# Kernel optimization log

Hardware: AMD Instinct MI355X
Metric: run time of the kernel (lower is better)

The kernel has to match this reference:

```python
import jax, jax.numpy as jnp
import numpy as np
from math import sqrt

SCALE = sqrt(512.0)  # max(key_size, attn_hidden_size, query_size) with scaled=True

def setup_inputs() -> dict:
    key = jax.random.key(0)
    k1, k2, k3, k4, k5 = jax.random.split(key, 5)
    B, T, S, M, N, H = 8, 512, 512, 512, 512, 128
    return {
        "query": jax.random.normal(k1, (B, T, M), dtype=jnp.float32),
        "keys": jax.random.normal(k2, (B, S, N), dtype=jnp.float32),
        "W1": jax.random.normal(k3, (N, H), dtype=jnp.float32),
        "W2": jax.random.normal(k4, (M, H), dtype=jnp.float32),
        "v": jax.random.normal(k5, (H,), dtype=jnp.float32),
    }

def reference(query, keys, W1, W2, v):
    # Project query and keys into attention hidden space
    x1 = jnp.einsum('btm,mh->bth', query, W2)   # (B,T,H)
    x2 = jnp.einsum('bsn,nh->bsh', keys, W1)    # (B,S,H)
    # Broadcast merge (op='add'), tanh activation, v-weighted reduction over H
    merged = jnp.tanh(x1[:, :, None, :] + x2[:, None, :, :])  # (B,T,S,H)
    score = jnp.einsum('btsh,h->bts', merged, v)
    return score / SCALE
```

## Files before the change

### kernel.cpp

```cpp
#include <hip/hip_runtime.h>
#include <hip/hip_fp16.h>


constexpr float SCALE_IN  = 2.8853900817779268f;
constexpr float INV_SCALE = 0.04419417382415922f;

__global__ __launch_bounds__(512) void proj_kernel(
    const float* __restrict__ q,  const float* __restrict__ w2,
    const float* __restrict__ ky, const float* __restrict__ w1,
    unsigned int* __restrict__ x1w, unsigned int* __restrict__ x2w) {
  __shared__ float As[32 * 64];
  __shared__ float Ws[64 * 128];

  int blk = blockIdx.x;
  const float* A; const float* W; unsigned int* O;
  if (blk < 128) { A = q;  W = w2; O = x1w; }
  else           { blk -= 128; A = ky; W = w1; O = x2w; }
  const int rbase = blk * 32;
  const int tid = threadIdx.x;

  const int rq = tid >> 5;
  const int hq = tid & 31;

  float acc[2][4];
#pragma unroll
  for (int r = 0; r < 2; ++r)
#pragma unroll
    for (int c = 0; c < 4; ++c) acc[r][c] = 0.0f;

  for (int kb = 0; kb < 512; kb += 64) {
    {
      const int arow = tid >> 4;
      const int kq4  = (tid & 15) * 4;
      *(float4*)(As + arow * 64 + kq4) =
          *(const float4*)(A + (size_t)(rbase + arow) * 512 + kb + kq4);
      const int wrow = tid >> 5;
      const int hq4  = (tid & 31) * 4;
#pragma unroll
      for (int p = 0; p < 4; ++p)
        *(float4*)(Ws + (wrow + 16 * p) * 128 + hq4) =
            *(const float4*)(W + (size_t)(kb + wrow + 16 * p) * 128 + hq4);
    }
    __syncthreads();
#pragma unroll 4
    for (int k4 = 0; k4 < 64; k4 += 4) {
      float a[2][4], w[4][4];
      *(float4*)a[0] = *(const float4*)(As + (2 * rq + 0) * 64 + k4);
      *(float4*)a[1] = *(const float4*)(As + (2 * rq + 1) * 64 + k4);
#pragma unroll
      for (int kk = 0; kk < 4; ++kk)
        *(float4*)w[kk] = *(const float4*)(Ws + (k4 + kk) * 128 + 4 * hq);
#pragma unroll
      for (int kk = 0; kk < 4; ++kk)
#pragma unroll
        for (int r = 0; r < 2; ++r)
#pragma unroll
          for (int c = 0; c < 4; ++c)
            acc[r][c] = fmaf(a[r][kk], w[kk][c], acc[r][c]);
    }
    __syncthreads();
  }

#pragma unroll
  for (int r = 0; r < 2; ++r) {
    unsigned int pk[4];
#pragma unroll
    for (int c = 0; c < 4; ++c) {
      const float z  = acc[r][c] * SCALE_IN;
      const float kf = rintf(z);
      const int   ki = (int)kf;
      const float em = __builtin_amdgcn_exp2f(z - kf);
      const __half hh = __float2half_rn(em);
      pk[c] = ((unsigned int)ki << 16) | (unsigned int)__half_as_ushort(hh);
    }
    *(uint4*)(O + (size_t)(rbase + 2 * rq + r) * 128 + 4 * hq) = *(uint4*)pk;
  }
}

__global__ __launch_bounds__(512) void score_kernel(
    const unsigned int* __restrict__ x1w, const unsigned int* __restrict__ x2w,
    const float* __restrict__ v, float* __restrict__ out) {
  __shared__ unsigned int x1l[128 * 64];
  __shared__ unsigned int x2l[128 * 64];

  const int tid   = threadIdx.x;
  const int b     = blockIdx.x >> 6;
  const int tile  = blockIdx.x & 63;
  const int tbase = (tile >> 3) * 64;
  const int sbase = (tile & 7) * 64;

  const uint4* x1g = (const uint4*)(x1w + (b * 512 + tbase) * 128);
  const uint4* x2g = (const uint4*)(x2w + (b * 512 + sbase) * 128);

  const int l  = tid & 63;
  const int wq = tid >> 6;
#pragma unroll
  for (int p = 0; p < 4; ++p) {
    const int row = (l & 31) + 32 * (p & 1);
    const int c4  = (l >> 5) + 2 * wq + 16 * (p >> 1);
    const uint4 a = x1g[row * 32 + c4];
    x1l[(4 * c4 + 0) * 64 + row] = a.x;
    x1l[(4 * c4 + 1) * 64 + row] = a.y;
    x1l[(4 * c4 + 2) * 64 + row] = a.z;
    x1l[(4 * c4 + 3) * 64 + row] = a.w;
    const uint4 c = x2g[row * 32 + c4];
    x2l[(4 * c4 + 0) * 64 + row] = c.x;
    x2l[(4 * c4 + 1) * 64 + row] = c.y;
    x2l[(4 * c4 + 2) * 64 + row] = c.z;
    x2l[(4 * c4 + 3) * 64 + row] = c.w;
  }
  __syncthreads();

  const int sg = tid & 15;
  const int tg = tid >> 4;

  float racc[2][4];
#pragma unroll
  for (int i = 0; i < 2; ++i)
#pragma unroll
    for (int j = 0; j < 4; ++j) racc[i][j] = 0.0f;
  float sv = 0.0f;

  for (int hg = 0; hg < 32; ++hg) {
    const int h0 = hg * 4;
    const float4 vq = *(const float4*)(v + h0);
    sv += (vq.x + vq.y) + (vq.z + vq.w);

    float emt[2][4]; int kt[2][4];
    float ems[4][4]; int ks[4][4];
#pragma unroll
    for (int qq = 0; qq < 4; ++qq) {
      const uint2 tp = *(const uint2*)(x1l + (h0 + qq) * 64 + 2 * tg);
      emt[0][qq] = __half2float(__ushort_as_half((unsigned short)tp.x));
      kt [0][qq] = ((int)tp.x) >> 16;
      emt[1][qq] = __half2float(__ushort_as_half((unsigned short)tp.y));
      kt [1][qq] = ((int)tp.y) >> 16;
      const uint4 sp = *(const uint4*)(x2l + (h0 + qq) * 64 + 4 * sg);
      ems[0][qq] = __half2float(__ushort_as_half((unsigned short)sp.x));
      ks [0][qq] = ((int)sp.x) >> 16;
      ems[1][qq] = __half2float(__ushort_as_half((unsigned short)sp.y));
      ks [1][qq] = ((int)sp.y) >> 16;
      ems[2][qq] = __half2float(__ushort_as_half((unsigned short)sp.z));
      ks [2][qq] = ((int)sp.z) >> 16;
      ems[3][qq] = __half2float(__ushort_as_half((unsigned short)sp.w));
      ks [3][qq] = ((int)sp.w) >> 16;
    }

#pragma unroll
    for (int i = 0; i < 2; ++i) {
#pragma unroll
      for (int j = 0; j < 4; ++j) {
        float e[4];
#pragma unroll
        for (int qq = 0; qq < 4; ++qq) {
          int kk = kt[i][qq] + ks[j][qq];
          kk = min(kk, 30);
          e[qq] = ldexpf(emt[i][qq] * ems[j][qq], kk);
        }
        const float a0 = e[0] + 1.0f, a1 = e[1] + 1.0f;
        const float a2 = e[2] + 1.0f, a3 = e[3] + 1.0f;
        const float p12 = a0 * a1, p34 = a2 * a3;
        float u1 = vq.x * a1; u1 = fmaf(vq.y, a0, u1);
        float u2 = vq.z * a3; u2 = fmaf(vq.w, a2, u2);
        float num = u1 * p34; num = fmaf(u2, p12, num);
        const float den = p12 * p34;
        racc[i][j] = fmaf(num, __builtin_amdgcn_rcpf(den), racc[i][j]);
      }
    }
  }

  const float c1 = sv * INV_SCALE;
  const float c2 = -2.0f * INV_SCALE;
#pragma unroll
  for (int i = 0; i < 2; ++i) {
    const int t = tbase + 2 * tg + i;
    float4 o;
    o.x = fmaf(racc[i][0], c2, c1);
    o.y = fmaf(racc[i][1], c2, c1);
    o.z = fmaf(racc[i][2], c2, c1);
    o.w = fmaf(racc[i][3], c2, c1);
    *(float4*)(out + (size_t)(b * 512 + t) * 512 + sbase + 4 * sg) = o;
  }
}

extern "C" void kernel_launch(void* const* d_in, const int* in_sizes, int n_in,
                              void* d_out, int out_size, void* d_ws, size_t ws_size,
                              hipStream_t stream) {
  const float* query = (const float*)d_in[0];
  const float* keys  = (const float*)d_in[1];
  const float* W1    = (const float*)d_in[2];
  const float* W2    = (const float*)d_in[3];
  const float* v     = (const float*)d_in[4];
  float* out = (float*)d_out;

  unsigned int* x1w = (unsigned int*)d_ws;
  unsigned int* x2w = x1w + 8 * 512 * 128;

  hipLaunchKernelGGL(proj_kernel, dim3(256), dim3(512), 0, stream,
                     query, W2, keys, W1, x1w, x2w);
  hipLaunchKernelGGL(score_kernel, dim3(512), dim3(512), 0, stream,
                     x1w, x2w, v, out);
}
```

Measured before the change: 145.7 us.

## Pack score math into float2 vectors and retile kernels to smaller blocks

```diff
diff --git a/kernel.cpp b/kernel.cpp
--- a/kernel.cpp
+++ b/kernel.cpp
@@ -2,25 +2,26 @@
 #include <hip/hip_fp16.h>
 
 
+typedef float vf2 __attribute__((ext_vector_type(2)));
+
 constexpr float SCALE_IN  = 2.8853900817779268f;
 constexpr float INV_SCALE = 0.04419417382415922f;
 
-__global__ __launch_bounds__(512) void proj_kernel(
+__global__ __launch_bounds__(256) void proj_kernel(
     const float* __restrict__ q,  const float* __restrict__ w2,
     const float* __restrict__ ky, const float* __restrict__ w1,
     unsigned int* __restrict__ x1w, unsigned int* __restrict__ x2w) {
-  __shared__ float As[32 * 64];
+  __shared__ float As[16 * 64];
   __shared__ float Ws[64 * 128];
 
   int blk = blockIdx.x;
   const float* A; const float* W; unsigned int* O;
-  if (blk < 128) { A = q;  W = w2; O = x1w; }
-  else           { blk -= 128; A = ky; W = w1; O = x2w; }
-  const int rbase = blk * 32;
+  if (blk < 256) { A = q;  W = w2; O = x1w; }
+  else           { blk -= 256; A = ky; W = w1; O = x2w; }
+  const int rbase = blk * 16;
   const int tid = threadIdx.x;
-
-  const int rq = tid >> 5;
-  const int hq = tid & 31;
+  const int hq  = tid & 31;
+  const int rg  = tid >> 5;
 
   float acc[2][4];
 #pragma unroll
@@ -31,22 +32,22 @@
   for (int kb = 0; kb < 512; kb += 64) {
     {
       const int arow = tid >> 4;
-      const int kq4  = (tid & 15) * 4;
-      *(float4*)(As + arow * 64 + kq4) =
-          *(const float4*)(A + (size_t)(rbase + arow) * 512 + kb + kq4);
-      const int wrow = tid >> 5;
-      const int hq4  = (tid & 31) * 4;
-#pragma unroll
-      for (int p = 0; p < 4; ++p)
-        *(float4*)(Ws + (wrow + 16 * p) * 128 + hq4) =
-            *(const float4*)(W + (size_t)(kb + wrow + 16 * p) * 128 + hq4);
+      const int k4   = (tid & 15) * 4;
+      *(float4*)(As + arow * 64 + k4) =
+          *(const float4*)(A + (size_t)(rbase + arow) * 512 + kb + k4);
+      const int hq4 = (tid & 31) * 4;
+      const int w0  = tid >> 5;
+#pragma unroll
+      for (int p = 0; p < 8; ++p)
+        *(float4*)(Ws + (w0 + 8 * p) * 128 + hq4) =
+            *(const float4*)(W + (size_t)(kb + w0 + 8 * p) * 128 + hq4);
     }
     __syncthreads();
 #pragma unroll 4
     for (int k4 = 0; k4 < 64; k4 += 4) {
       float a[2][4], w[4][4];
-      *(float4*)a[0] = *(const float4*)(As + (2 * rq + 0) * 64 + k4);
-      *(float4*)a[1] = *(const float4*)(As + (2 * rq + 1) * 64 + k4);
+      *(float4*)a[0] = *(const float4*)(As + (2 * rg + 0) * 64 + k4);
+      *(float4*)a[1] = *(const float4*)(As + (2 * rg + 1) * 64 + k4);
 #pragma unroll
       for (int kk = 0; kk < 4; ++kk)
         *(float4*)w[kk] = *(const float4*)(Ws + (k4 + kk) * 128 + 4 * hq);
@@ -70,101 +71,107 @@
       const float kf = rintf(z);
       const int   ki = (int)kf;
       const float em = __builtin_amdgcn_exp2f(z - kf);
-      const __half hh = __float2half_rn(em);
-      pk[c] = ((unsigned int)ki << 16) | (unsigned int)__half_as_ushort(hh);
-    }
-    *(uint4*)(O + (size_t)(rbase + 2 * rq + r) * 128 + 4 * hq) = *(uint4*)pk;
+      pk[c] = ((unsigned int)ki << 16) |
+              (unsigned int)__half_as_ushort(__float2half_rn(em));
+    }
+    *(uint4*)(O + (size_t)(rbase + 2 * rg + r) * 128 + 4 * hq) = *(uint4*)pk;
   }
 }
 
-__global__ __launch_bounds__(512) void score_kernel(
+__global__ __launch_bounds__(256) void score_kernel(
     const unsigned int* __restrict__ x1w, const unsigned int* __restrict__ x2w,
     const float* __restrict__ v, float* __restrict__ out) {
-  __shared__ unsigned int x1l[128 * 64];
-  __shared__ unsigned int x2l[128 * 64];
+  __shared__ unsigned int x1l[64 * 64];
+  __shared__ unsigned int x2l[64 * 32];
 
   const int tid   = threadIdx.x;
-  const int b     = blockIdx.x >> 6;
-  const int tile  = blockIdx.x & 63;
-  const int tbase = (tile >> 3) * 64;
-  const int sbase = (tile & 7) * 64;
-
-  const uint4* x1g = (const uint4*)(x1w + (b * 512 + tbase) * 128);
-  const uint4* x2g = (const uint4*)(x2w + (b * 512 + sbase) * 128);
-
-  const int l  = tid & 63;
-  const int wq = tid >> 6;
-#pragma unroll
-  for (int p = 0; p < 4; ++p) {
-    const int row = (l & 31) + 32 * (p & 1);
-    const int c4  = (l >> 5) + 2 * wq + 16 * (p >> 1);
-    const uint4 a = x1g[row * 32 + c4];
-    x1l[(4 * c4 + 0) * 64 + row] = a.x;
-    x1l[(4 * c4 + 1) * 64 + row] = a.y;
-    x1l[(4 * c4 + 2) * 64 + row] = a.z;
-    x1l[(4 * c4 + 3) * 64 + row] = a.w;
-    const uint4 c = x2g[row * 32 + c4];
-    x2l[(4 * c4 + 0) * 64 + row] = c.x;
-    x2l[(4 * c4 + 1) * 64 + row] = c.y;
-    x2l[(4 * c4 + 2) * 64 + row] = c.z;
-    x2l[(4 * c4 + 3) * 64 + row] = c.w;
-  }
-  __syncthreads();
+  const int b     = blockIdx.x >> 7;
+  const int tile  = blockIdx.x & 127;
+  const int tbase = (tile >> 4) * 64;
+  const int sbase = (tile & 15) * 32;
 
   const int sg = tid & 15;
   const int tg = tid >> 4;
 
-  float racc[2][4];
-#pragma unroll
-  for (int i = 0; i < 2; ++i)
-#pragma unroll
-    for (int j = 0; j < 4; ++j) racc[i][j] = 0.0f;
+  const int st_t = tid >> 2, st_q = tid & 3;
+  const int s2_t = tid >> 3, s2_q = tid & 7;
+
+  const uint4* x1g = (const uint4*)x1w + (size_t)(b * 512 + tbase) * 32;
+  const uint4* x2g = (const uint4*)x2w + (size_t)(b * 512 + sbase) * 32;
+
+  vf2 racc[4];
+#pragma unroll
+  for (int i = 0; i < 4; ++i) racc[i] = (vf2){0.0f, 0.0f};
   float sv = 0.0f;
 
-  for (int hg = 0; hg < 32; ++hg) {
-    const int h0 = hg * 4;
-    const float4 vq = *(const float4*)(v + h0);
-    sv += (vq.x + vq.y) + (vq.z + vq.w);
-
-    float emt[2][4]; int kt[2][4];
-    float ems[4][4]; int ks[4][4];
-#pragma unroll
-    for (int qq = 0; qq < 4; ++qq) {
-      const uint2 tp = *(const uint2*)(x1l + (h0 + qq) * 64 + 2 * tg);
-      emt[0][qq] = __half2float(__ushort_as_half((unsigned short)tp.x));
-      kt [0][qq] = ((int)tp.x) >> 16;
-      emt[1][qq] = __half2float(__ushort_as_half((unsigned short)tp.y));
-      kt [1][qq] = ((int)tp.y) >> 16;
-      const uint4 sp = *(const uint4*)(x2l + (h0 + qq) * 64 + 4 * sg);
-      ems[0][qq] = __half2float(__ushort_as_half((unsigned short)sp.x));
-      ks [0][qq] = ((int)sp.x) >> 16;
-      ems[1][qq] = __half2float(__ushort_as_half((unsigned short)sp.y));
-      ks [1][qq] = ((int)sp.y) >> 16;
-      ems[2][qq] = __half2float(__ushort_as_half((unsigned short)sp.z));
-      ks [2][qq] = ((int)sp.z) >> 16;
-      ems[3][qq] = __half2float(__ushort_as_half((unsigned short)sp.w));
-      ks [3][qq] = ((int)sp.w) >> 16;
-    }
-
-#pragma unroll
-    for (int i = 0; i < 2; ++i) {
-#pragma unroll
-      for (int j = 0; j < 4; ++j) {
-        float e[4];
+  for (int c = 0; c < 2; ++c) {
+    if (c) __syncthreads();
+#pragma unroll
+    for (int p = 0; p < 4; ++p) {
+      const int hq = st_q + 4 * p;
+      const uint4 a = x1g[(size_t)st_t * 32 + 16 * c + hq];
+      x1l[(4 * hq + 0) * 64 + st_t] = a.x;
+      x1l[(4 * hq + 1) * 64 + st_t] = a.y;
+      x1l[(4 * hq + 2) * 64 + st_t] = a.z;
+      x1l[(4 * hq + 3) * 64 + st_t] = a.w;
+    }
+#pragma unroll
+    for (int p = 0; p < 2; ++p) {
+      const int hq = s2_q + 8 * p;
+      const uint4 a = x2g[(size_t)s2_t * 32 + 16 * c + hq];
+      x2l[(4 * hq + 0) * 32 + s2_t] = a.x;
+      x2l[(4 * hq + 1) * 32 + s2_t] = a.y;
+      x2l[(4 * hq + 2) * 32 + s2_t] = a.z;
+      x2l[(4 * hq + 3) * 32 + s2_t] = a.w;
+    }
+    __syncthreads();
+
+    for (int hg = 0; hg < 16; ++hg) {
+      const int h0 = 4 * hg;
+      const float4 vq = *(const float4*)(v + 64 * c + h0);
+      sv += (vq.x + vq.y) + (vq.z + vq.w);
+
+      float emt[4][4]; int kt[4][4];
+      vf2 ems[4]; int ks[4][2];
+#pragma unroll
+      for (int qq = 0; qq < 4; ++qq) {
+        const uint4 tp = *(const uint4*)(x1l + (h0 + qq) * 64 + 4 * tg);
+        emt[qq][0] = __half2float(__ushort_as_half((unsigned short)tp.x));
+        kt [qq][0] = ((int)tp.x) >> 16;
+        emt[qq][1] = __half2float(__ushort_as_half((unsigned short)tp.y));
+        kt [qq][1] = ((int)tp.y) >> 16;
+        emt[qq][2] = __half2float(__ushort_as_half((unsigned short)tp.z));
+        kt [qq][2] = ((int)tp.z) >> 16;
+        emt[qq][3] = __half2float(__ushort_as_half((unsigned short)tp.w));
+        kt [qq][3] = ((int)tp.w) >> 16;
+        const uint2 sp = *(const uint2*)(x2l + (h0 + qq) * 32 + 2 * sg);
+        ems[qq].x = __half2float(__ushort_as_half((unsigned short)sp.x));
+        ems[qq].y = __half2float(__ushort_as_half((unsigned short)sp.y));
+        ks [qq][0] = ((int)sp.x) >> 16;
+        ks [qq][1] = ((int)sp.y) >> 16;
+      }
+
+#pragma unroll
+      for (int i = 0; i < 4; ++i) {
+        vf2 Aq[4];
 #pragma unroll
         for (int qq = 0; qq < 4; ++qq) {
-          int kk = kt[i][qq] + ks[j][qq];
-          kk = min(kk, 30);
-          e[qq] = ldexpf(emt[i][qq] * ems[j][qq], kk);
+          const int k0 = min(kt[qq][i] + ks[qq][0], 30);
+          const int k1 = min(kt[qq][i] + ks[qq][1], 30);
+          const vf2 m = emt[qq][i] * ems[qq];
+          vf2 e; e.x = ldexpf(m.x, k0); e.y = ldexpf(m.y, k1);
+          Aq[qq] = e + 1.0f;
         }
-        const float a0 = e[0] + 1.0f, a1 = e[1] + 1.0f;
-        const float a2 = e[2] + 1.0f, a3 = e[3] + 1.0f;
-        const float p12 = a0 * a1, p34 = a2 * a3;
-        float u1 = vq.x * a1; u1 = fmaf(vq.y, a0, u1);
-        float u2 = vq.z * a3; u2 = fmaf(vq.w, a2, u2);
-        float num = u1 * p34; num = fmaf(u2, p12, num);
-        const float den = p12 * p34;
-        racc[i][j] = fmaf(num, __builtin_amdgcn_rcpf(den), racc[i][j]);
+        const vf2 N01 = vq.x * Aq[1] + vq.y * Aq[0];
+        const vf2 N23 = vq.z * Aq[3] + vq.w * Aq[2];
+        const vf2 D01 = Aq[0] * Aq[1];
+        const vf2 D23 = Aq[2] * Aq[3];
+        const vf2 NUM = N01 * D23 + N23 * D01;
+        const vf2 DEN = D01 * D23;
+        vf2 R;
+        R.x = __builtin_amdgcn_rcpf(DEN.x);
+        R.y = __builtin_amdgcn_rcpf(DEN.y);
+        racc[i] += NUM * R;
       }
     }
   }
@@ -172,14 +179,9 @@
   const float c1 = sv * INV_SCALE;
   const float c2 = -2.0f * INV_SCALE;
 #pragma unroll
-  for (int i = 0; i < 2; ++i) {
-    const int t = tbase + 2 * tg + i;
-    float4 o;
-    o.x = fmaf(racc[i][0], c2, c1);
-    o.y = fmaf(racc[i][1], c2, c1);
-    o.z = fmaf(racc[i][2], c2, c1);
-    o.w = fmaf(racc[i][3], c2, c1);
-    *(float4*)(out + (size_t)(b * 512 + t) * 512 + sbase + 4 * sg) = o;
+  for (int i = 0; i < 4; ++i) {
+    const vf2 o = c2 * racc[i] + c1;
+    *(vf2*)(out + (size_t)(b * 512 + tbase + 4 * tg + i) * 512 + sbase + 2 * sg) = o;
   }
 }
 
@@ -196,8 +198,8 @@
   unsigned int* x1w = (unsigned int*)d_ws;
   unsigned int* x2w = x1w + 8 * 512 * 128;
 
-  hipLaunchKernelGGL(proj_kernel, dim3(256), dim3(512), 0, stream,
+  hipLaunchKernelGGL(proj_kernel, dim3(512), dim3(256), 0, stream,
                      query, W2, keys, W1, x1w, x2w);
-  hipLaunchKernelGGL(score_kernel, dim3(512), dim3(512), 0, stream,
+  hipLaunchKernelGGL(score_kernel, dim3(1024), dim3(256), 0, stream,
                      x1w, x2w, v, out);
 }
```

After: 145.7 us. Within noise of the previous version (+0.0%).
